# Kernel optimization log

Hardware: AMD Instinct MI355X
Metric: run time of the kernel (lower is better)

## Reference

```python
import jax, jax.numpy as jnp
import numpy as np

MIDC = 128
HEADS = 4
HEADC = MIDC // HEADS
EPS = 1e-5


def _layernorm(x, w, b):
    # Faithful to the custom torch LayerNorm: unbiased std (ddof=1) and (std + eps) in denominator.
    mean = jnp.mean(x, axis=-1, keepdims=True)
    std = jnp.std(x, axis=-1, keepdims=True, ddof=1)
    return w * ((x - mean) / (std + EPS)) + b


def setup_inputs() -> dict:
    key = jax.random.key(0)
    ks = jax.random.split(key, 8)
    B, C, D, H, W = 2, MIDC, 16, 64, 64
    s = 1.0 / np.sqrt(C)
    return {
        "x": jax.random.normal(ks[0], (B, C, D, H, W), dtype=jnp.float32),
        "qkv_w": jax.random.normal(ks[1], (3 * C, C), dtype=jnp.float32) * s,
        "qkv_b": jnp.zeros((3 * C,), dtype=jnp.float32),
        "o1_w": jax.random.normal(ks[2], (C, C), dtype=jnp.float32) * s,
        "o1_b": jnp.zeros((C,), dtype=jnp.float32),
        "o2_w": jax.random.normal(ks[3], (C, C), dtype=jnp.float32) * s,
        "o2_b": jnp.zeros((C,), dtype=jnp.float32),
        "kln_w": jnp.ones((HEADS, 1, HEADC), dtype=jnp.float32),
        "kln_b": jnp.zeros((HEADS, 1, HEADC), dtype=jnp.float32),
        "vln_w": jnp.ones((HEADS, 1, HEADC), dtype=jnp.float32),
        "vln_b": jnp.zeros((HEADS, 1, HEADC), dtype=jnp.float32),
    }


def reference(x, qkv_w, qkv_b, o1_w, o1_b, o2_w, o2_b, kln_w, kln_b, vln_w, vln_b):
    B, C, D, H, W = x.shape
    heads, headc = HEADS, HEADC
    bias = x
    # 1x1x1 Conv3d == pointwise linear over channel dim
    qkv = jnp.einsum('bcdhw,oc->bdhwo', x, qkv_w) + qkv_b          # [B,D,H,W,3C]
    qkv = qkv.reshape(B * D, H * W, heads, 3 * headc)
    qkv = qkv.transpose(0, 2, 1, 3)                                 # [BD,heads,HW,3hc]
    q, k, v = jnp.split(qkv, 3, axis=-1)                            # each [BD,heads,HW,hc]
    k = _layernorm(k, kln_w, kln_b)
    v = _layernorm(v, vln_w, vln_b)
    # linear attention: (K^T V) then Q (K^T V)
    kv = jnp.einsum('bhnc,bhnd->bhcd', k, v) / (H * W)              # [BD,heads,hc,hc]
    v = jnp.einsum('bhnc,bhcd->bhnd', q, kv)                        # [BD,heads,HW,hc]
    v = v.transpose(0, 2, 1, 3).reshape(B, D, H, W, C)
    ret = v.transpose(0, 4, 1, 2, 3) + bias                         # [B,C,D,H,W]
    h = jnp.einsum('bcdhw,oc->bodhw', ret, o1_w) + o1_b[None, :, None, None, None]
    h = jax.nn.gelu(h, approximate=False)
    out = jnp.einsum('bcdhw,oc->bodhw', h, o2_w) + o2_b[None, :, None, None, None]
    return out + bias
```

## Files before the change

kernel.cpp:

```cpp
#include <hip/hip_runtime.h>
#include <cmath>

typedef float  f32x4  __attribute__((ext_vector_type(4)));
typedef __bf16 bf16x8 __attribute__((ext_vector_type(8)));
typedef __bf16 bf16x4 __attribute__((ext_vector_type(4)));
typedef __bf16 bf16x2 __attribute__((ext_vector_type(2)));

#define MFMA16(acc, a, b) (acc) = __builtin_amdgcn_mfma_f32_16x16x32_bf16((a), (b), (acc), 0, 0, 0)


__device__ __forceinline__ int swz(int row, int colByte){ return row*256 + (colByte ^ ((row & 7) << 4)); }
__device__ __forceinline__ int swzP(int row, int colByte){ return row*128 + (colByte ^ ((row & 7) << 4)); }

__device__ __forceinline__ void loadx(float* sx, const float* __restrict__ xb, int t){
  int p = t & 63, cg = t >> 6;
  const float* col = xb + p;
  #pragma unroll
  for (int i = 0; i < 4; ++i)
    #pragma unroll
    for (int j = 0; j < 8; ++j)
      sx[i*8 + j] = col[(cg*8 + i*32 + j) * 65536];
}
__device__ __forceinline__ void writex(const float* sx, char* ldsX, int t){
  int p = t & 63, cg = t >> 6;
  #pragma unroll
  for (int i = 0; i < 4; ++i){
    bf16x8 u;
    #pragma unroll
    for (int j = 0; j < 8; ++j) u[j] = (__bf16)sx[i*8 + j];
    *(bf16x8*)(ldsX + swz(p, cg*16 + i*64)) = u;
  }
}

__global__ __launch_bounds__(256) void wprep(const float* __restrict__ qkv_w,
                                             const float* __restrict__ o1w,
                                             const float* __restrict__ o2w,
                                             __bf16* __restrict__ w16){
  int e = (blockIdx.x * 256 + threadIdx.x) * 4;
  const float* src; int off;
  if (e < 49152)      { src = qkv_w; off = e; }
  else if (e < 65536) { src = o1w;   off = e - 49152; }
  else                { src = o2w;   off = e - 65536; }
  f32x4 v = *(const f32x4*)(src + off);
  bf16x4 o;
  #pragma unroll
  for (int r = 0; r < 4; ++r) o[r] = (__bf16)v[r];
  *(bf16x4*)(w16 + e) = o;
}

__global__ __launch_bounds__(256, 3) void k1_kv(
    const float* __restrict__ x, const __bf16* __restrict__ w16, const float* __restrict__ qkv_b,
    const float* __restrict__ klw, const float* __restrict__ klb,
    const float* __restrict__ vlw, const float* __restrict__ vlb,
    __bf16* __restrict__ part){
  __shared__ char ldsX[16384];
  __shared__ char tS[4][8192];
  int t = threadIdx.x, lane = t & 63, w = t >> 6, l15 = lane & 15, l4 = lane >> 4;
  int bx = blockIdx.x, bd = bx >> 5, b = bd >> 4, d = bd & 15;
  const float* xb = x + (size_t)b*8388608 + d*4096 + (bx & 31)*128;
  char* ks = tS[w];
  char* vs = tS[w] + 4096;
  f32x4 kv[2][2] = {};

  float sx[32];
  loadx(sx, xb, t);
  writex(sx, ldsX, t);
  __syncthreads();

  #pragma unroll
  for (int ch = 0; ch < 2; ++ch){
    if (ch == 0){
      loadx(sx, xb + 64, t);
    } else {
      __syncthreads();
      writex(sx, ldsX, t);
      __syncthreads();
    }
    #pragma unroll
    for (int ph = 0; ph < 2; ++ph){
      int po = 96*w + 32 + 32*ph;
      f32x4 acc[2][4] = {};
      #pragma unroll
      for (int kf = 0; kf < 4; ++kf){
        bf16x8 a0 = *(const bf16x8*)(w16 + (po + l15)*128 + kf*32 + l4*8);
        bf16x8 a1 = *(const bf16x8*)(w16 + (po + 16 + l15)*128 + kf*32 + l4*8);
        bf16x8 bn0 = *(const bf16x8*)(ldsX + swz(l15,      kf*64 + l4*16));
        bf16x8 bn1 = *(const bf16x8*)(ldsX + swz(16 + l15, kf*64 + l4*16));
        bf16x8 bn2 = *(const bf16x8*)(ldsX + swz(32 + l15, kf*64 + l4*16));
        bf16x8 bn3 = *(const bf16x8*)(ldsX + swz(48 + l15, kf*64 + l4*16));
        MFMA16(acc[0][0], a0, bn0); MFMA16(acc[0][1], a0, bn1);
        MFMA16(acc[0][2], a0, bn2); MFMA16(acc[0][3], a0, bn3);
        MFMA16(acc[1][0], a1, bn0); MFMA16(acc[1][1], a1, bn1);
        MFMA16(acc[1][2], a1, bn2); MFMA16(acc[1][3], a1, bn3);
      }
      const float* lwp = (ph ? vlw : klw) + 32*w;
      const float* lbp = (ph ? vlb : klb) + 32*w;
      f32x4 b0  = *(const f32x4*)(qkv_b + po + l4*4);
      f32x4 b1  = *(const f32x4*)(qkv_b + po + 16 + l4*4);
      f32x4 lw0 = *(const f32x4*)(lwp + l4*4), lw1 = *(const f32x4*)(lwp + 16 + l4*4);
      f32x4 lb0 = *(const f32x4*)(lbp + l4*4), lb1 = *(const f32x4*)(lbp + 16 + l4*4);
      char* dst = ph ? vs : ks;
      #pragma unroll
      for (int n = 0; n < 4; ++n){
        f32x4 v0 = acc[0][n] + b0;
        f32x4 v1 = acc[1][n] + b1;
        float s1 = v0[0]+v0[1]+v0[2]+v0[3] + v1[0]+v1[1]+v1[2]+v1[3];
        float s2 = v0[0]*v0[0]+v0[1]*v0[1]+v0[2]*v0[2]+v0[3]*v0[3]
                 + v1[0]*v1[0]+v1[1]*v1[1]+v1[2]*v1[2]+v1[3]*v1[3];
        s1 += __shfl_xor(s1, 16); s2 += __shfl_xor(s2, 16);
        s1 += __shfl_xor(s1, 32); s2 += __shfl_xor(s2, 32);
        float m   = s1 * (1.f/32.f);
        float var = fmaxf((s2 - 32.f*m*m) * (1.f/31.f), 0.f);
        float inv = 1.f / (sqrtf(var) + 1e-5f);
        v0 = (v0 - m) * inv * lw0 + lb0;
        v1 = (v1 - m) * inv * lw1 + lb1;
        int pB = (16*n + l15) * 2;
        #pragma unroll
        for (int r = 0; r < 4; ++r){
          *(__bf16*)(dst + swzP(l4*4 + r, pB))      = (__bf16)v0[r];
          *(__bf16*)(dst + swzP(16 + l4*4 + r, pB)) = (__bf16)v1[r];
        }
      }
    }
    #pragma unroll
    for (int kf = 0; kf < 2; ++kf){
      bf16x8 av0 = *(const bf16x8*)(vs + swzP(l15,      kf*64 + l4*16));
      bf16x8 av1 = *(const bf16x8*)(vs + swzP(16 + l15, kf*64 + l4*16));
      bf16x8 bk0 = *(const bf16x8*)(ks + swzP(l15,      kf*64 + l4*16));
      bf16x8 bk1 = *(const bf16x8*)(ks + swzP(16 + l15, kf*64 + l4*16));
      MFMA16(kv[0][0], av0, bk0); MFMA16(kv[0][1], av0, bk1);
      MFMA16(kv[1][0], av1, bk0); MFMA16(kv[1][1], av1, bk1);
    }
  }

  __bf16* pb = part + (size_t)bx*4096 + w*1024;
  #pragma unroll
  for (int m = 0; m < 2; ++m)
    #pragma unroll
    for (int n = 0; n < 2; ++n)
      #pragma unroll
      for (int r = 0; r < 4; ++r)
        pb[(16*m + l4*4 + r)*32 + 16*n + l15] = (__bf16)kv[m][n][r];
}

__global__ __launch_bounds__(256) void k15_reduce(const __bf16* __restrict__ part,
                                                  __bf16* __restrict__ kvt){
  int bx = blockIdx.x, t = threadIdx.x;
  int bd = bx >> 3, seg = bx & 7;
  int e = seg * 512 + t * 2;
  float s0 = 0.f, s1 = 0.f;
  #pragma unroll
  for (int sub = 0; sub < 32; ++sub){
    bf16x2 p = *(const bf16x2*)(part + (size_t)(bd * 32 + sub) * 4096 + e);
    s0 += (float)p[0]; s1 += (float)p[1];
  }
  bf16x2 o; o[0] = (__bf16)(s0 * (1.f / 4096.f)); o[1] = (__bf16)(s1 * (1.f / 4096.f));
  *(bf16x2*)(kvt + bd * 4096 + e) = o;
}

__global__ __launch_bounds__(256, 3) void k2_main(
    const float* __restrict__ x, const __bf16* __restrict__ w16, const float* __restrict__ qkv_b,
    const float* __restrict__ o1b, const float* __restrict__ o2b,
    const __bf16* __restrict__ kvt, float* __restrict__ out){
  __shared__ char ldsX2[2][16384];
  __shared__ char wk[16384];
  int t = threadIdx.x, lane = t & 63, w = t >> 6, l15 = lane & 15, l4 = lane >> 4;
  int bx = blockIdx.x;
  const __bf16* w1 = w16 + 49152;
  const __bf16* w2 = w16 + 65536;
  int oo = 32 * w;

  float sx[32];
  {
    int tt = bx * 2, bd = tt >> 6;
    const float* xb0 = x + (size_t)(bd >> 4)*8388608 + (bd & 15)*4096 + (tt & 63)*64;
    loadx(sx, xb0, t);
    writex(sx, ldsX2[0], t);
  }
  __syncthreads();

  #pragma unroll
  for (int ti = 0; ti < 2; ++ti){
    int tt = bx * 2 + ti, bd = tt >> 6;
    size_t gofs = (size_t)(bd >> 4)*8388608 + (bd & 15)*4096 + (tt & 63)*64;
    float* ob = out + gofs;
    char* lx = ldsX2[ti];
    if (ti == 0){
      int t2 = tt + 1, bd2 = t2 >> 6;
      const float* xb1 = x + (size_t)(bd2 >> 4)*8388608 + (bd2 & 15)*4096 + (t2 & 63)*64;
      loadx(sx, xb1, t);
    } else {
      __syncthreads();
    }

    {
      f32x4 acc[2][4] = {};
      #pragma unroll
      for (int kf = 0; kf < 4; ++kf){
        bf16x8 a0 = *(const bf16x8*)(w16 + (96*w + l15)*128 + kf*32 + l4*8);
        bf16x8 a1 = *(const bf16x8*)(w16 + (96*w + 16 + l15)*128 + kf*32 + l4*8);
        bf16x8 bn0 = *(const bf16x8*)(lx + swz(l15,      kf*64 + l4*16));
        bf16x8 bn1 = *(const bf16x8*)(lx + swz(16 + l15, kf*64 + l4*16));
        bf16x8 bn2 = *(const bf16x8*)(lx + swz(32 + l15, kf*64 + l4*16));
        bf16x8 bn3 = *(const bf16x8*)(lx + swz(48 + l15, kf*64 + l4*16));
        MFMA16(acc[0][0], a0, bn0); MFMA16(acc[0][1], a0, bn1);
        MFMA16(acc[0][2], a0, bn2); MFMA16(acc[0][3], a0, bn3);
        MFMA16(acc[1][0], a1, bn0); MFMA16(acc[1][1], a1, bn1);
        MFMA16(acc[1][2], a1, bn2); MFMA16(acc[1][3], a1, bn3);
      }
      #pragma unroll
      for (int m = 0; m < 2; ++m){
        f32x4 qb = *(const f32x4*)(qkv_b + 96*w + 16*m + l4*4);
        int cB = (oo + 16*m + l4*4) * 2;
        #pragma unroll
        for (int n = 0; n < 4; ++n){
          bf16x4 pk;
          #pragma unroll
          for (int r = 0; r < 4; ++r) pk[r] = (__bf16)(acc[m][n][r] + qb[r]);
          *(bf16x4*)(wk + swz(16*n + l15, cB)) = pk;
        }
      }
    }
    {
      const __bf16* kvh = kvt + ((size_t)bd*4 + w)*1024;
      bf16x8 ka0 = *(const bf16x8*)(kvh + l15*32 + l4*8);
      bf16x8 ka1 = *(const bf16x8*)(kvh + (16 + l15)*32 + l4*8);
      f32x4 acc[2][4] = {};
      #pragma unroll
      for (int n = 0; n < 4; ++n){
        bf16x8 bq = *(const bf16x8*)(wk + swz(16*n + l15, oo*2 + l4*16));
        MFMA16(acc[0][n], ka0, bq);
        MFMA16(acc[1][n], ka1, bq);
      }
      #pragma unroll
      for (int m = 0; m < 2; ++m){
        int cB = (oo + 16*m + l4*4) * 2;
        #pragma unroll
        for (int n = 0; n < 4; ++n){
          bf16x4 xv = *(const bf16x4*)(lx + swz(16*n + l15, cB));
          bf16x4 pk;
          #pragma unroll
          for (int r = 0; r < 4; ++r) pk[r] = (__bf16)(acc[m][n][r] + (float)xv[r]);
          *(bf16x4*)(wk + swz(16*n + l15, cB)) = pk;
        }
      }
    }
    if (ti == 0) writex(sx, ldsX2[1], t);
    __syncthreads();

    f32x4 acc1[2][4] = {};
    #pragma unroll
    for (int kf = 0; kf < 4; ++kf){
      bf16x8 a0 = *(const bf16x8*)(w1 + (oo + l15)*128 + kf*32 + l4*8);
      bf16x8 a1 = *(const bf16x8*)(w1 + (oo + 16 + l15)*128 + kf*32 + l4*8);
      bf16x8 bn0 = *(const bf16x8*)(wk + swz(l15,      kf*64 + l4*16));
      bf16x8 bn1 = *(const bf16x8*)(wk + swz(16 + l15, kf*64 + l4*16));
      bf16x8 bn2 = *(const bf16x8*)(wk + swz(32 + l15, kf*64 + l4*16));
      bf16x8 bn3 = *(const bf16x8*)(wk + swz(48 + l15, kf*64 + l4*16));
      MFMA16(acc1[0][0], a0, bn0); MFMA16(acc1[0][1], a0, bn1);
      MFMA16(acc1[0][2], a0, bn2); MFMA16(acc1[0][3], a0, bn3);
      MFMA16(acc1[1][0], a1, bn0); MFMA16(acc1[1][1], a1, bn1);
      MFMA16(acc1[1][2], a1, bn2); MFMA16(acc1[1][3], a1, bn3);
    }
    __syncthreads();
    #pragma unroll
    for (int m = 0; m < 2; ++m){
      f32x4 bb = *(const f32x4*)(o1b + oo + 16*m + l4*4);
      int cB = (oo + 16*m + l4*4) * 2;
      #pragma unroll
      for (int n = 0; n < 4; ++n){
        bf16x4 pk;
        #pragma unroll
        for (int r = 0; r < 4; ++r){
          float v = acc1[m][n][r] + bb[r];
          float z = v * (1.5957691216f + 0.0713548164f * v * v);
          float g = v / (1.f + __expf(-z));
          pk[r] = (__bf16)g;
        }
        *(bf16x4*)(wk + swz(16*n + l15, cB)) = pk;
      }
    }
    __syncthreads();

    f32x4 acc2[2][4] = {};
    #pragma unroll
    for (int kf = 0; kf < 4; ++kf){
      bf16x8 a0 = *(const bf16x8*)(w2 + (oo + l15)*128 + kf*32 + l4*8);
      bf16x8 a1 = *(const bf16x8*)(w2 + (oo + 16 + l15)*128 + kf*32 + l4*8);
      bf16x8 bn0 = *(const bf16x8*)(wk + swz(l15,      kf*64 + l4*16));
      bf16x8 bn1 = *(const bf16x8*)(wk + swz(16 + l15, kf*64 + l4*16));
      bf16x8 bn2 = *(const bf16x8*)(wk + swz(32 + l15, kf*64 + l4*16));
      bf16x8 bn3 = *(const bf16x8*)(wk + swz(48 + l15, kf*64 + l4*16));
      MFMA16(acc2[0][0], a0, bn0); MFMA16(acc2[0][1], a0, bn1);
      MFMA16(acc2[0][2], a0, bn2); MFMA16(acc2[0][3], a0, bn3);
      MFMA16(acc2[1][0], a1, bn0); MFMA16(acc2[1][1], a1, bn1);
      MFMA16(acc2[1][2], a1, bn2); MFMA16(acc2[1][3], a1, bn3);
    }
    #pragma unroll
    for (int m = 0; m < 2; ++m){
      int c0 = oo + 16*m + l4*4;
      f32x4 bb = *(const f32x4*)(o2b + c0);
      #pragma unroll
      for (int n = 0; n < 4; ++n){
        bf16x4 xv = *(const bf16x4*)(lx + swz(16*n + l15, c0*2));
        #pragma unroll
        for (int r = 0; r < 4; ++r)
          ob[(size_t)(c0 + r)*65536 + 16*n + l15] = acc2[m][n][r] + bb[r] + (float)xv[r];
      }
    }
  }
}

extern "C" void kernel_launch(void* const* d_in, const int* in_sizes, int n_in,
                              void* d_out, int out_size, void* d_ws, size_t ws_size,
                              hipStream_t stream){
  const float* x     = (const float*)d_in[0];
  const float* qkv_w = (const float*)d_in[1];
  const float* qkv_b = (const float*)d_in[2];
  const float* o1w   = (const float*)d_in[3];
  const float* o1b   = (const float*)d_in[4];
  const float* o2w   = (const float*)d_in[5];
  const float* o2b   = (const float*)d_in[6];
  const float* klw   = (const float*)d_in[7];
  const float* klb   = (const float*)d_in[8];
  const float* vlw   = (const float*)d_in[9];
  const float* vlb   = (const float*)d_in[10];

  __bf16* part = (__bf16*)d_ws;
  __bf16* kvt  = (__bf16*)((char*)d_ws + 8388608);
  __bf16* w16  = (__bf16*)((char*)d_ws + 8650752);

  wprep<<<80, 256, 0, stream>>>(qkv_w, o1w, o2w, w16);
  k1_kv<<<1024, 256, 0, stream>>>(x, w16, qkv_b, klw, klb, vlw, vlb, part);
  k15_reduce<<<256, 256, 0, stream>>>(part, kvt);
  k2_main<<<1024, 256, 0, stream>>>(x, w16, qkv_b, o1b, o2b, kvt, (float*)d_out);
}
```

Baseline: 91.02 us.

## Replace partial-sum reduction kernel with fp32 atomics and halve per-block tiles

The KV partial products are now accumulated straight into an fp32 workspace with atomicAdd, which removes the separate reduction kernel and the bf16 partial buffer. A memset is added to zero that workspace. Both main kernels now process one 64-pixel tile per block over 2048 blocks instead of two tiles over 1024. Dropping the in-block double-buffered x prefetch and sharing the x LDS buffer for V lowers LDS use, so occupancy hints rise from 3 to 5. The costs are atomic contention (64 blocks per bd slice) and losing the prefetch overlap inside each block.

```diff
diff --git a/kernel.cpp b/kernel.cpp
--- a/kernel.cpp
+++ b/kernel.cpp
@@ -4,7 +4,6 @@
 typedef float  f32x4  __attribute__((ext_vector_type(4)));
 typedef __bf16 bf16x8 __attribute__((ext_vector_type(8)));
 typedef __bf16 bf16x4 __attribute__((ext_vector_type(4)));
-typedef __bf16 bf16x2 __attribute__((ext_vector_type(2)));
 
 #define MFMA16(acc, a, b) (acc) = __builtin_amdgcn_mfma_f32_16x16x32_bf16((a), (b), (acc), 0, 0, 0)
 
@@ -48,265 +47,244 @@
   *(bf16x4*)(w16 + e) = o;
 }
 
-__global__ __launch_bounds__(256, 3) void k1_kv(
+__global__ __launch_bounds__(256, 5) void k1_kv(
     const float* __restrict__ x, const __bf16* __restrict__ w16, const float* __restrict__ qkv_b,
     const float* __restrict__ klw, const float* __restrict__ klb,
     const float* __restrict__ vlw, const float* __restrict__ vlb,
-    __bf16* __restrict__ part){
+    float* __restrict__ kvacc){
   __shared__ char ldsX[16384];
-  __shared__ char tS[4][8192];
+  __shared__ char ksS[4][4096];
   int t = threadIdx.x, lane = t & 63, w = t >> 6, l15 = lane & 15, l4 = lane >> 4;
-  int bx = blockIdx.x, bd = bx >> 5, b = bd >> 4, d = bd & 15;
-  const float* xb = x + (size_t)b*8388608 + d*4096 + (bx & 31)*128;
-  char* ks = tS[w];
-  char* vs = tS[w] + 4096;
-  f32x4 kv[2][2] = {};
+  int bx = blockIdx.x, bd = bx >> 6, b = bd >> 4, d = bd & 15;
+  const float* xb = x + (size_t)b*8388608 + d*4096 + (bx & 63)*64;
 
   float sx[32];
   loadx(sx, xb, t);
   writex(sx, ldsX, t);
   __syncthreads();
 
-  #pragma unroll
-  for (int ch = 0; ch < 2; ++ch){
-    if (ch == 0){
-      loadx(sx, xb + 64, t);
-    } else {
-      __syncthreads();
-      writex(sx, ldsX, t);
-      __syncthreads();
-    }
-    #pragma unroll
-    for (int ph = 0; ph < 2; ++ph){
-      int po = 96*w + 32 + 32*ph;
-      f32x4 acc[2][4] = {};
-      #pragma unroll
-      for (int kf = 0; kf < 4; ++kf){
-        bf16x8 a0 = *(const bf16x8*)(w16 + (po + l15)*128 + kf*32 + l4*8);
-        bf16x8 a1 = *(const bf16x8*)(w16 + (po + 16 + l15)*128 + kf*32 + l4*8);
-        bf16x8 bn0 = *(const bf16x8*)(ldsX + swz(l15,      kf*64 + l4*16));
-        bf16x8 bn1 = *(const bf16x8*)(ldsX + swz(16 + l15, kf*64 + l4*16));
-        bf16x8 bn2 = *(const bf16x8*)(ldsX + swz(32 + l15, kf*64 + l4*16));
-        bf16x8 bn3 = *(const bf16x8*)(ldsX + swz(48 + l15, kf*64 + l4*16));
-        MFMA16(acc[0][0], a0, bn0); MFMA16(acc[0][1], a0, bn1);
-        MFMA16(acc[0][2], a0, bn2); MFMA16(acc[0][3], a0, bn3);
-        MFMA16(acc[1][0], a1, bn0); MFMA16(acc[1][1], a1, bn1);
-        MFMA16(acc[1][2], a1, bn2); MFMA16(acc[1][3], a1, bn3);
-      }
-      const float* lwp = (ph ? vlw : klw) + 32*w;
-      const float* lbp = (ph ? vlb : klb) + 32*w;
-      f32x4 b0  = *(const f32x4*)(qkv_b + po + l4*4);
-      f32x4 b1  = *(const f32x4*)(qkv_b + po + 16 + l4*4);
-      f32x4 lw0 = *(const f32x4*)(lwp + l4*4), lw1 = *(const f32x4*)(lwp + 16 + l4*4);
-      f32x4 lb0 = *(const f32x4*)(lbp + l4*4), lb1 = *(const f32x4*)(lbp + 16 + l4*4);
-      char* dst = ph ? vs : ks;
-      #pragma unroll
-      for (int n = 0; n < 4; ++n){
-        f32x4 v0 = acc[0][n] + b0;
-        f32x4 v1 = acc[1][n] + b1;
-        float s1 = v0[0]+v0[1]+v0[2]+v0[3] + v1[0]+v1[1]+v1[2]+v1[3];
-        float s2 = v0[0]*v0[0]+v0[1]*v0[1]+v0[2]*v0[2]+v0[3]*v0[3]
-                 + v1[0]*v1[0]+v1[1]*v1[1]+v1[2]*v1[2]+v1[3]*v1[3];
-        s1 += __shfl_xor(s1, 16); s2 += __shfl_xor(s2, 16);
-        s1 += __shfl_xor(s1, 32); s2 += __shfl_xor(s2, 32);
-        float m   = s1 * (1.f/32.f);
-        float var = fmaxf((s2 - 32.f*m*m) * (1.f/31.f), 0.f);
-        float inv = 1.f / (sqrtf(var) + 1e-5f);
-        v0 = (v0 - m) * inv * lw0 + lb0;
-        v1 = (v1 - m) * inv * lw1 + lb1;
+  char* ks = ksS[w];
+  f32x4 accv[2][4];
+  #pragma unroll
+  for (int ph = 0; ph < 2; ++ph){
+    int po = 96*w + 32 + 32*ph;
+    f32x4 acc[2][4] = {};
+    #pragma unroll
+    for (int kf = 0; kf < 4; ++kf){
+      bf16x8 a0 = *(const bf16x8*)(w16 + (po + l15)*128 + kf*32 + l4*8);
+      bf16x8 a1 = *(const bf16x8*)(w16 + (po + 16 + l15)*128 + kf*32 + l4*8);
+      bf16x8 bn0 = *(const bf16x8*)(ldsX + swz(l15,      kf*64 + l4*16));
+      bf16x8 bn1 = *(const bf16x8*)(ldsX + swz(16 + l15, kf*64 + l4*16));
+      bf16x8 bn2 = *(const bf16x8*)(ldsX + swz(32 + l15, kf*64 + l4*16));
+      bf16x8 bn3 = *(const bf16x8*)(ldsX + swz(48 + l15, kf*64 + l4*16));
+      MFMA16(acc[0][0], a0, bn0); MFMA16(acc[0][1], a0, bn1);
+      MFMA16(acc[0][2], a0, bn2); MFMA16(acc[0][3], a0, bn3);
+      MFMA16(acc[1][0], a1, bn0); MFMA16(acc[1][1], a1, bn1);
+      MFMA16(acc[1][2], a1, bn2); MFMA16(acc[1][3], a1, bn3);
+    }
+    const float* lwp = (ph ? vlw : klw) + 32*w;
+    const float* lbp = (ph ? vlb : klb) + 32*w;
+    f32x4 b0  = *(const f32x4*)(qkv_b + po + l4*4);
+    f32x4 b1  = *(const f32x4*)(qkv_b + po + 16 + l4*4);
+    f32x4 lw0 = *(const f32x4*)(lwp + l4*4), lw1 = *(const f32x4*)(lwp + 16 + l4*4);
+    f32x4 lb0 = *(const f32x4*)(lbp + l4*4), lb1 = *(const f32x4*)(lbp + 16 + l4*4);
+    #pragma unroll
+    for (int n = 0; n < 4; ++n){
+      f32x4 v0 = acc[0][n] + b0;
+      f32x4 v1 = acc[1][n] + b1;
+      float s1 = v0[0]+v0[1]+v0[2]+v0[3] + v1[0]+v1[1]+v1[2]+v1[3];
+      float s2 = v0[0]*v0[0]+v0[1]*v0[1]+v0[2]*v0[2]+v0[3]*v0[3]
+               + v1[0]*v1[0]+v1[1]*v1[1]+v1[2]*v1[2]+v1[3]*v1[3];
+      s1 += __shfl_xor(s1, 16); s2 += __shfl_xor(s2, 16);
+      s1 += __shfl_xor(s1, 32); s2 += __shfl_xor(s2, 32);
+      float m   = s1 * (1.f/32.f);
+      float var = fmaxf((s2 - 32.f*m*m) * (1.f/31.f), 0.f);
+      float inv = 1.f / (sqrtf(var) + 1e-5f);
+      v0 = (v0 - m) * inv * lw0 + lb0;
+      v1 = (v1 - m) * inv * lw1 + lb1;
+      if (ph == 0){
         int pB = (16*n + l15) * 2;
         #pragma unroll
         for (int r = 0; r < 4; ++r){
-          *(__bf16*)(dst + swzP(l4*4 + r, pB))      = (__bf16)v0[r];
-          *(__bf16*)(dst + swzP(16 + l4*4 + r, pB)) = (__bf16)v1[r];
+          *(__bf16*)(ks + swzP(l4*4 + r, pB))      = (__bf16)v0[r];
+          *(__bf16*)(ks + swzP(16 + l4*4 + r, pB)) = (__bf16)v1[r];
         }
+      } else {
+        accv[0][n] = v0; accv[1][n] = v1;
       }
     }
-    #pragma unroll
-    for (int kf = 0; kf < 2; ++kf){
-      bf16x8 av0 = *(const bf16x8*)(vs + swzP(l15,      kf*64 + l4*16));
-      bf16x8 av1 = *(const bf16x8*)(vs + swzP(16 + l15, kf*64 + l4*16));
-      bf16x8 bk0 = *(const bf16x8*)(ks + swzP(l15,      kf*64 + l4*16));
-      bf16x8 bk1 = *(const bf16x8*)(ks + swzP(16 + l15, kf*64 + l4*16));
-      MFMA16(kv[0][0], av0, bk0); MFMA16(kv[0][1], av0, bk1);
-      MFMA16(kv[1][0], av1, bk0); MFMA16(kv[1][1], av1, bk1);
-    }
-  }
-
-  __bf16* pb = part + (size_t)bx*4096 + w*1024;
+  }
+  __syncthreads();
+  char* vs = ldsX + w * 4096;
+  #pragma unroll
+  for (int n = 0; n < 4; ++n){
+    int pB = (16*n + l15) * 2;
+    #pragma unroll
+    for (int r = 0; r < 4; ++r){
+      *(__bf16*)(vs + swzP(l4*4 + r, pB))      = (__bf16)accv[0][n][r];
+      *(__bf16*)(vs + swzP(16 + l4*4 + r, pB)) = (__bf16)accv[1][n][r];
+    }
+  }
+  f32x4 kv[2][2] = {};
+  #pragma unroll
+  for (int kf = 0; kf < 2; ++kf){
+    bf16x8 av0 = *(const bf16x8*)(vs + swzP(l15,      kf*64 + l4*16));
+    bf16x8 av1 = *(const bf16x8*)(vs + swzP(16 + l15, kf*64 + l4*16));
+    bf16x8 bk0 = *(const bf16x8*)(ks + swzP(l15,      kf*64 + l4*16));
+    bf16x8 bk1 = *(const bf16x8*)(ks + swzP(16 + l15, kf*64 + l4*16));
+    MFMA16(kv[0][0], av0, bk0); MFMA16(kv[0][1], av0, bk1);
+    MFMA16(kv[1][0], av1, bk0); MFMA16(kv[1][1], av1, bk1);
+  }
+  float* kh = kvacc + ((size_t)bd*4 + w)*1024;
   #pragma unroll
   for (int m = 0; m < 2; ++m)
     #pragma unroll
     for (int n = 0; n < 2; ++n)
       #pragma unroll
       for (int r = 0; r < 4; ++r)
-        pb[(16*m + l4*4 + r)*32 + 16*n + l15] = (__bf16)kv[m][n][r];
-}
-
-__global__ __launch_bounds__(256) void k15_reduce(const __bf16* __restrict__ part,
-                                                  __bf16* __restrict__ kvt){
-  int bx = blockIdx.x, t = threadIdx.x;
-  int bd = bx >> 3, seg = bx & 7;
-  int e = seg * 512 + t * 2;
-  float s0 = 0.f, s1 = 0.f;
-  #pragma unroll
-  for (int sub = 0; sub < 32; ++sub){
-    bf16x2 p = *(const bf16x2*)(part + (size_t)(bd * 32 + sub) * 4096 + e);
-    s0 += (float)p[0]; s1 += (float)p[1];
-  }
-  bf16x2 o; o[0] = (__bf16)(s0 * (1.f / 4096.f)); o[1] = (__bf16)(s1 * (1.f / 4096.f));
-  *(bf16x2*)(kvt + bd * 4096 + e) = o;
-}
-
-__global__ __launch_bounds__(256, 3) void k2_main(
+        atomicAdd(kh + (16*m + l4*4 + r)*32 + 16*n + l15, kv[m][n][r] * (1.f/4096.f));
+}
+
+__global__ __launch_bounds__(256, 5) void k2_main(
     const float* __restrict__ x, const __bf16* __restrict__ w16, const float* __restrict__ qkv_b,
     const float* __restrict__ o1b, const float* __restrict__ o2b,
-    const __bf16* __restrict__ kvt, float* __restrict__ out){
-  __shared__ char ldsX2[2][16384];
+    const float* __restrict__ kvacc, float* __restrict__ out){
+  __shared__ char lx[16384];
   __shared__ char wk[16384];
   int t = threadIdx.x, lane = t & 63, w = t >> 6, l15 = lane & 15, l4 = lane >> 4;
-  int bx = blockIdx.x;
+  int bx = blockIdx.x, bd = bx >> 6, b = bd >> 4, d = bd & 15;
+  size_t gofs = (size_t)b*8388608 + d*4096 + (bx & 63)*64;
+  const float* xb = x + gofs;
+  float* ob = out + gofs;
   const __bf16* w1 = w16 + 49152;
   const __bf16* w2 = w16 + 65536;
   int oo = 32 * w;
 
   float sx[32];
+  loadx(sx, xb, t);
+  const float* kvh = kvacc + ((size_t)bd*4 + w)*1024;
+  f32x4 ql0 = *(const f32x4*)(kvh + l15*32 + l4*8);
+  f32x4 qh0 = *(const f32x4*)(kvh + l15*32 + l4*8 + 4);
+  f32x4 ql1 = *(const f32x4*)(kvh + (16 + l15)*32 + l4*8);
+  f32x4 qh1 = *(const f32x4*)(kvh + (16 + l15)*32 + l4*8 + 4);
+  writex(sx, lx, t);
+  bf16x8 ka0, ka1;
+  #pragma unroll
+  for (int j = 0; j < 4; ++j){
+    ka0[j] = (__bf16)ql0[j]; ka0[j+4] = (__bf16)qh0[j];
+    ka1[j] = (__bf16)ql1[j]; ka1[j+4] = (__bf16)qh1[j];
+  }
+  __syncthreads();
+
   {
-    int tt = bx * 2, bd = tt >> 6;
-    const float* xb0 = x + (size_t)(bd >> 4)*8388608 + (bd & 15)*4096 + (tt & 63)*64;
-    loadx(sx, xb0, t);
-    writex(sx, ldsX2[0], t);
-  }
-  __syncthreads();
-
-  #pragma unroll
-  for (int ti = 0; ti < 2; ++ti){
-    int tt = bx * 2 + ti, bd = tt >> 6;
-    size_t gofs = (size_t)(bd >> 4)*8388608 + (bd & 15)*4096 + (tt & 63)*64;
-    float* ob = out + gofs;
-    char* lx = ldsX2[ti];
-    if (ti == 0){
-      int t2 = tt + 1, bd2 = t2 >> 6;
-      const float* xb1 = x + (size_t)(bd2 >> 4)*8388608 + (bd2 & 15)*4096 + (t2 & 63)*64;
-      loadx(sx, xb1, t);
-    } else {
-      __syncthreads();
-    }
-
-    {
-      f32x4 acc[2][4] = {};
-      #pragma unroll
-      for (int kf = 0; kf < 4; ++kf){
-        bf16x8 a0 = *(const bf16x8*)(w16 + (96*w + l15)*128 + kf*32 + l4*8);
-        bf16x8 a1 = *(const bf16x8*)(w16 + (96*w + 16 + l15)*128 + kf*32 + l4*8);
-        bf16x8 bn0 = *(const bf16x8*)(lx + swz(l15,      kf*64 + l4*16));
-        bf16x8 bn1 = *(const bf16x8*)(lx + swz(16 + l15, kf*64 + l4*16));
-        bf16x8 bn2 = *(const bf16x8*)(lx + swz(32 + l15, kf*64 + l4*16));
-        bf16x8 bn3 = *(const bf16x8*)(lx + swz(48 + l15, kf*64 + l4*16));
-        MFMA16(acc[0][0], a0, bn0); MFMA16(acc[0][1], a0, bn1);
-        MFMA16(acc[0][2], a0, bn2); MFMA16(acc[0][3], a0, bn3);
-        MFMA16(acc[1][0], a1, bn0); MFMA16(acc[1][1], a1, bn1);
-        MFMA16(acc[1][2], a1, bn2); MFMA16(acc[1][3], a1, bn3);
-      }
-      #pragma unroll
-      for (int m = 0; m < 2; ++m){
-        f32x4 qb = *(const f32x4*)(qkv_b + 96*w + 16*m + l4*4);
-        int cB = (oo + 16*m + l4*4) * 2;
-        #pragma unroll
-        for (int n = 0; n < 4; ++n){
-          bf16x4 pk;
-          #pragma unroll
-          for (int r = 0; r < 4; ++r) pk[r] = (__bf16)(acc[m][n][r] + qb[r]);
-          *(bf16x4*)(wk + swz(16*n + l15, cB)) = pk;
-        }
-      }
-    }
-    {
-      const __bf16* kvh = kvt + ((size_t)bd*4 + w)*1024;
-      bf16x8 ka0 = *(const bf16x8*)(kvh + l15*32 + l4*8);
-      bf16x8 ka1 = *(const bf16x8*)(kvh + (16 + l15)*32 + l4*8);
-      f32x4 acc[2][4] = {};
-      #pragma unroll
-      for (int n = 0; n < 4; ++n){
-        bf16x8 bq = *(const bf16x8*)(wk + swz(16*n + l15, oo*2 + l4*16));
-        MFMA16(acc[0][n], ka0, bq);
-        MFMA16(acc[1][n], ka1, bq);
-      }
-      #pragma unroll
-      for (int m = 0; m < 2; ++m){
-        int cB = (oo + 16*m + l4*4) * 2;
-        #pragma unroll
-        for (int n = 0; n < 4; ++n){
-          bf16x4 xv = *(const bf16x4*)(lx + swz(16*n + l15, cB));
-          bf16x4 pk;
-          #pragma unroll
-          for (int r = 0; r < 4; ++r) pk[r] = (__bf16)(acc[m][n][r] + (float)xv[r]);
-          *(bf16x4*)(wk + swz(16*n + l15, cB)) = pk;
-        }
-      }
-    }
-    if (ti == 0) writex(sx, ldsX2[1], t);
-    __syncthreads();
-
-    f32x4 acc1[2][4] = {};
+    f32x4 acc[2][4] = {};
     #pragma unroll
     for (int kf = 0; kf < 4; ++kf){
-      bf16x8 a0 = *(const bf16x8*)(w1 + (oo + l15)*128 + kf*32 + l4*8);
-      bf16x8 a1 = *(const bf16x8*)(w1 + (oo + 16 + l15)*128 + kf*32 + l4*8);
-      bf16x8 bn0 = *(const bf16x8*)(wk + swz(l15,      kf*64 + l4*16));
-      bf16x8 bn1 = *(const bf16x8*)(wk + swz(16 + l15, kf*64 + l4*16));
-      bf16x8 bn2 = *(const bf16x8*)(wk + swz(32 + l15, kf*64 + l4*16));
-      bf16x8 bn3 = *(const bf16x8*)(wk + swz(48 + l15, kf*64 + l4*16));
-      MFMA16(acc1[0][0], a0, bn0); MFMA16(acc1[0][1], a0, bn1);
-      MFMA16(acc1[0][2], a0, bn2); MFMA16(acc1[0][3], a0, bn3);
-      MFMA16(acc1[1][0], a1, bn0); MFMA16(acc1[1][1], a1, bn1);
-      MFMA16(acc1[1][2], a1, bn2); MFMA16(acc1[1][3], a1, bn3);
-    }
-    __syncthreads();
+      bf16x8 a0 = *(const bf16x8*)(w16 + (96*w + l15)*128 + kf*32 + l4*8);
+      bf16x8 a1 = *(const bf16x8*)(w16 + (96*w + 16 + l15)*128 + kf*32 + l4*8);
+      bf16x8 bn0 = *(const bf16x8*)(lx + swz(l15,      kf*64 + l4*16));
+      bf16x8 bn1 = *(const bf16x8*)(lx + swz(16 + l15, kf*64 + l4*16));
+      bf16x8 bn2 = *(const bf16x8*)(lx + swz(32 + l15, kf*64 + l4*16));
+      bf16x8 bn3 = *(const bf16x8*)(lx + swz(48 + l15, kf*64 + l4*16));
+      MFMA16(acc[0][0], a0, bn0); MFMA16(acc[0][1], a0, bn1);
+      MFMA16(acc[0][2], a0, bn2); MFMA16(acc[0][3], a0, bn3);
+      MFMA16(acc[1][0], a1, bn0); MFMA16(acc[1][1], a1, bn1);
+      MFMA16(acc[1][2], a1, bn2); MFMA16(acc[1][3], a1, bn3);
+    }
     #pragma unroll
     for (int m = 0; m < 2; ++m){
-      f32x4 bb = *(const f32x4*)(o1b + oo + 16*m + l4*4);
+      f32x4 qb = *(const f32x4*)(qkv_b + 96*w + 16*m + l4*4);
       int cB = (oo + 16*m + l4*4) * 2;
       #pragma unroll
       for (int n = 0; n < 4; ++n){
         bf16x4 pk;
         #pragma unroll
-        for (int r = 0; r < 4; ++r){
-          float v = acc1[m][n][r] + bb[r];
-          float z = v * (1.5957691216f + 0.0713548164f * v * v);
-          float g = v / (1.f + __expf(-z));
-          pk[r] = (__bf16)g;
-        }
+        for (int r = 0; r < 4; ++r) pk[r] = (__bf16)(acc[m][n][r] + qb[r]);
         *(bf16x4*)(wk + swz(16*n + l15, cB)) = pk;
       }
     }
-    __syncthreads();
-
-    f32x4 acc2[2][4] = {};
-    #pragma unroll
-    for (int kf = 0; kf < 4; ++kf){
-      bf16x8 a0 = *(const bf16x8*)(w2 + (oo + l15)*128 + kf*32 + l4*8);
-      bf16x8 a1 = *(const bf16x8*)(w2 + (oo + 16 + l15)*128 + kf*32 + l4*8);
-      bf16x8 bn0 = *(const bf16x8*)(wk + swz(l15,      kf*64 + l4*16));
-      bf16x8 bn1 = *(const bf16x8*)(wk + swz(16 + l15, kf*64 + l4*16));
-      bf16x8 bn2 = *(const bf16x8*)(wk + swz(32 + l15, kf*64 + l4*16));
-      bf16x8 bn3 = *(const bf16x8*)(wk + swz(48 + l15, kf*64 + l4*16));
-      MFMA16(acc2[0][0], a0, bn0); MFMA16(acc2[0][1], a0, bn1);
-      MFMA16(acc2[0][2], a0, bn2); MFMA16(acc2[0][3], a0, bn3);
-      MFMA16(acc2[1][0], a1, bn0); MFMA16(acc2[1][1], a1, bn1);
-      MFMA16(acc2[1][2], a1, bn2); MFMA16(acc2[1][3], a1, bn3);
+  }
+  {
+    f32x4 acc[2][4] = {};
+    #pragma unroll
+    for (int n = 0; n < 4; ++n){
+      bf16x8 bq = *(const bf16x8*)(wk + swz(16*n + l15, oo*2 + l4*16));
+      MFMA16(acc[0][n], ka0, bq);
+      MFMA16(acc[1][n], ka1, bq);
     }
     #pragma unroll
     for (int m = 0; m < 2; ++m){
-      int c0 = oo + 16*m + l4*4;
-      f32x4 bb = *(const f32x4*)(o2b + c0);
+      int cB = (oo + 16*m + l4*4) * 2;
       #pragma unroll
       for (int n = 0; n < 4; ++n){
-        bf16x4 xv = *(const bf16x4*)(lx + swz(16*n + l15, c0*2));
+        bf16x4 xv = *(const bf16x4*)(lx + swz(16*n + l15, cB));
+        bf16x4 pk;
         #pragma unroll
-        for (int r = 0; r < 4; ++r)
-          ob[(size_t)(c0 + r)*65536 + 16*n + l15] = acc2[m][n][r] + bb[r] + (float)xv[r];
+        for (int r = 0; r < 4; ++r) pk[r] = (__bf16)(acc[m][n][r] + (float)xv[r]);
+        *(bf16x4*)(wk + swz(16*n + l15, cB)) = pk;
       }
+    }
+  }
+  __syncthreads();
+
+  f32x4 acc1[2][4] = {};
+  #pragma unroll
+  for (int kf = 0; kf < 4; ++kf){
+    bf16x8 a0 = *(const bf16x8*)(w1 + (oo + l15)*128 + kf*32 + l4*8);
+    bf16x8 a1 = *(const bf16x8*)(w1 + (oo + 16 + l15)*128 + kf*32 + l4*8);
+    bf16x8 bn0 = *(const bf16x8*)(wk + swz(l15,      kf*64 + l4*16));
+    bf16x8 bn1 = *(const bf16x8*)(wk + swz(16 + l15, kf*64 + l4*16));
+    bf16x8 bn2 = *(const bf16x8*)(wk + swz(32 + l15, kf*64 + l4*16));
+    bf16x8 bn3 = *(const bf16x8*)(wk + swz(48 + l15, kf*64 + l4*16));
+    MFMA16(acc1[0][0], a0, bn0); MFMA16(acc1[0][1], a0, bn1);
+    MFMA16(acc1[0][2], a0, bn2); MFMA16(acc1[0][3], a0, bn3);
+    MFMA16(acc1[1][0], a1, bn0); MFMA16(acc1[1][1], a1, bn1);
+    MFMA16(acc1[1][2], a1, bn2); MFMA16(acc1[1][3], a1, bn3);
+  }
+  __syncthreads();
+  #pragma unroll
+  for (int m = 0; m < 2; ++m){
+    f32x4 bb = *(const f32x4*)(o1b + oo + 16*m + l4*4);
+    int cB = (oo + 16*m + l4*4) * 2;
+    #pragma unroll
+    for (int n = 0; n < 4; ++n){
+      bf16x4 pk;
+      #pragma unroll
+      for (int r = 0; r < 4; ++r){
+        float v = acc1[m][n][r] + bb[r];
+        float z = v * (1.5957691216f + 0.0713548164f * v * v);
+        float g = v / (1.f + __expf(-z));
+        pk[r] = (__bf16)g;
+      }
+      *(bf16x4*)(wk + swz(16*n + l15, cB)) = pk;
+    }
+  }
+  __syncthreads();
+
+  f32x4 acc2[2][4] = {};
+  #pragma unroll
+  for (int kf = 0; kf < 4; ++kf){
+    bf16x8 a0 = *(const bf16x8*)(w2 + (oo + l15)*128 + kf*32 + l4*8);
+    bf16x8 a1 = *(const bf16x8*)(w2 + (oo + 16 + l15)*128 + kf*32 + l4*8);
+    bf16x8 bn0 = *(const bf16x8*)(wk + swz(l15,      kf*64 + l4*16));
+    bf16x8 bn1 = *(const bf16x8*)(wk + swz(16 + l15, kf*64 + l4*16));
+    bf16x8 bn2 = *(const bf16x8*)(wk + swz(32 + l15, kf*64 + l4*16));
+    bf16x8 bn3 = *(const bf16x8*)(wk + swz(48 + l15, kf*64 + l4*16));
+    MFMA16(acc2[0][0], a0, bn0); MFMA16(acc2[0][1], a0, bn1);
+    MFMA16(acc2[0][2], a0, bn2); MFMA16(acc2[0][3], a0, bn3);
+    MFMA16(acc2[1][0], a1, bn0); MFMA16(acc2[1][1], a1, bn1);
+    MFMA16(acc2[1][2], a1, bn2); MFMA16(acc2[1][3], a1, bn3);
+  }
+  #pragma unroll
+  for (int m = 0; m < 2; ++m){
+    int c0 = oo + 16*m + l4*4;
+    f32x4 bb = *(const f32x4*)(o2b + c0);
+    #pragma unroll
+    for (int n = 0; n < 4; ++n){
+      bf16x4 xv = *(const bf16x4*)(lx + swz(16*n + l15, c0*2));
+      #pragma unroll
+      for (int r = 0; r < 4; ++r)
+        ob[(size_t)(c0 + r)*65536 + 16*n + l15] = acc2[m][n][r] + bb[r] + (float)xv[r];
     }
   }
 }
@@ -326,12 +304,11 @@
   const float* vlw   = (const float*)d_in[9];
   const float* vlb   = (const float*)d_in[10];
 
-  __bf16* part = (__bf16*)d_ws;
-  __bf16* kvt  = (__bf16*)((char*)d_ws + 8388608);
-  __bf16* w16  = (__bf16*)((char*)d_ws + 8650752);
-
+  float*  kvacc = (float*)d_ws;
+  __bf16* w16   = (__bf16*)((char*)d_ws + 524288);
+
+  hipMemsetAsync(kvacc, 0, (size_t)32 * 4096 * 4, stream);
   wprep<<<80, 256, 0, stream>>>(qkv_w, o1w, o2w, w16);
-  k1_kv<<<1024, 256, 0, stream>>>(x, w16, qkv_b, klw, klb, vlw, vlb, part);
-  k15_reduce<<<256, 256, 0, stream>>>(part, kvt);
-  k2_main<<<1024, 256, 0, stream>>>(x, w16, qkv_b, o1b, o2b, kvt, (float*)d_out);
-}
+  k1_kv<<<2048, 256, 0, stream>>>(x, w16, qkv_b, klw, klb, vlw, vlb, kvacc);
+  k2_main<<<2048, 256, 0, stream>>>(x, w16, qkv_b, o1b, o2b, kvacc, (float*)d_out);
+}
```

After: 106.9 us. 1.17x slower.
